# Optimization experiments

Hardware: AMD Instinct MI355X
Metric: run time of the kernel (lower is better)

Reference implementation:

```python
import jax, jax.numpy as jnp
import numpy as np

B, T, N, D = 16, 16, 256, 384  # batch, timesteps, patches, feature dim
QDIM = 384                      # query_dim
TEMP = 1.0                      # temperature
TOPK = 16                       # topk_k
EPS = 1e-8


def setup_inputs() -> dict:
    key = jax.random.key(0)
    k1, k2, k3, k4, k5, k6 = jax.random.split(key, 6)
    queries = jax.random.normal(k1, (B, T, QDIM), dtype=jnp.float32)
    patch_features = jax.random.normal(k2, (B, T, N, D), dtype=jnp.float32)
    # encoder.query_input_proj: Linear(query_dim -> D)
    W_in = jax.random.normal(k3, (QDIM, D), dtype=jnp.float32) / np.sqrt(QDIM)
    b_in = jax.random.normal(k4, (D,), dtype=jnp.float32) * 0.01
    # encoder.query_output_proj: Linear(D -> dino_dim)
    W_out = jax.random.normal(k5, (D, QDIM), dtype=jnp.float32) / np.sqrt(D)
    b_out = jax.random.normal(k6, (QDIM,), dtype=jnp.float32) * 0.01
    return {"queries": queries, "patch_features": patch_features,
            "W_in": W_in, "b_in": b_in, "W_out": W_out, "b_out": b_out}


def reference(queries, patch_features, W_in, b_in, W_out, b_out):
    # q_proj: [B,T,D]
    q_proj = jnp.einsum('btq,qd->btd', queries, W_in) + b_in
    # scores: [B,T,N]
    scores = jnp.einsum('btd,btnd->btn', q_proj, patch_features) / TEMP
    attn = jax.nn.softmax(scores, axis=-1)
    # top-k hard mask + renormalize
    k = min(TOPK, N)
    vals, idx = jax.lax.top_k(attn, k)                     # [B,T,k]
    bi = jnp.arange(B)[:, None, None]
    ti = jnp.arange(T)[None, :, None]
    attn_hard = jnp.zeros_like(attn).at[bi, ti, idx].set(vals)
    attn = attn_hard / (attn_hard.sum(axis=-1, keepdims=True) + EPS)
    # weighted sum over patches: [B,T,D]
    out = jnp.einsum('btn,btnd->btd', attn, patch_features)
    out = jnp.einsum('btd,dq->btq', out, W_out) + b_out    # [B,T,QDIM]
    return out
```

## Files before the change

### kernel.cpp

```cpp
#include <hip/hip_runtime.h>
#include <math.h>

#define B_  16
#define T_  16
#define N_  256
#define D_  384
#define Q_  384
#define K_  16
#define BT_ (B_ * T_)

__global__ __launch_bounds__(1024, 4)
void fused_kernel(const float* __restrict__ queries,
                  const float* __restrict__ patch,
                  const float* __restrict__ W_in,
                  const float* __restrict__ b_in,
                  const float* __restrict__ W_out,
                  const float* __restrict__ b_out,
                  float* __restrict__ out)
{
    const int bt   = blockIdx.x;
    const int tid  = threadIdx.x;
    const int lane = tid & 63;
    const int wave = tid >> 6;

    __shared__ __align__(16) float s_q[Q_];
    __shared__ __align__(16) float s_qp[D_];
    __shared__ float s_sc[N_];
    __shared__ int   s_cnt4[N_][4];
    __shared__ float s_red[4];
    __shared__ float s_red2[4][2];
    __shared__ float s_w[K_];
    __shared__ int   s_ix[K_];
    __shared__ float s_part[2 * D_];
    __shared__ float s_od[D_];

    const float* __restrict__ ptile = patch + (size_t)bt * N_ * D_;

    if (tid < Q_) s_q[tid] = queries[(size_t)bt * Q_ + tid];
    __syncthreads();

    const int g  = lane >> 4;
    const int sl = lane & 15;
    const int n0 = wave * 4 + g;

    float4 A[6], Bu[6];

#define LOADROW(dst, it) {                                                     \
        const float* pr = ptile + (size_t)(n0 + (it) * 64) * D_;               \
        _Pragma("unroll")                                                      \
        for (int c = 0; c < 6; ++c)                                            \
            dst[c] = *reinterpret_cast<const float4*>(pr + c * 64 + 4 * sl); }

#define DOTSTORE(src, it) {                                                    \
        float p = 0.f;                                                         \
        _Pragma("unroll")                                                      \
        for (int c = 0; c < 6; ++c)                                            \
            p += src[c].x * qv[c].x + src[c].y * qv[c].y                       \
               + src[c].z * qv[c].z + src[c].w * qv[c].w;                      \
        _Pragma("unroll")                                                      \
        for (int off = 8; off; off >>= 1) p += __shfl_xor(p, off, 16);         \
        if (sl == 0) s_sc[n0 + (it) * 64] = p; }

    LOADROW(A, 0)
    LOADROW(Bu, 1)
    __builtin_amdgcn_sched_barrier(0);

    if (tid < 2 * D_) {
        const int half = tid >= D_;
        const int d    = tid - half * D_;
        const int q0   = half * (Q_ / 2);
        float a0 = 0.f, a1 = 0.f, a2 = 0.f, a3 = 0.f;
        #pragma unroll 4
        for (int q = q0; q < q0 + Q_ / 2; q += 4) {
            a0 += s_q[q]     * W_in[(size_t)(q)     * D_ + d];
            a1 += s_q[q + 1] * W_in[(size_t)(q + 1) * D_ + d];
            a2 += s_q[q + 2] * W_in[(size_t)(q + 2) * D_ + d];
            a3 += s_q[q + 3] * W_in[(size_t)(q + 3) * D_ + d];
        }
        s_part[tid] = (a0 + a1) + (a2 + a3);
    }
    __syncthreads();
    if (tid < D_) s_qp[tid] = s_part[tid] + s_part[tid + D_] + b_in[tid];
    __syncthreads();

    {
        const float4* s_qp4 = reinterpret_cast<const float4*>(s_qp);
        float4 qv[6];
        #pragma unroll
        for (int c = 0; c < 6; ++c) qv[c] = s_qp4[c * 16 + sl];

        DOTSTORE(A, 0)
        LOADROW(A, 2)
        DOTSTORE(Bu, 1)
        LOADROW(Bu, 3)
        DOTSTORE(A, 2)
        DOTSTORE(Bu, 3)
    }
#undef LOADROW
#undef DOTSTORE
    __syncthreads();

    if (tid < N_) {
        float v = s_sc[tid];
        #pragma unroll
        for (int off = 32; off; off >>= 1) v = fmaxf(v, __shfl_xor(v, off));
        if (lane == 0) s_red[wave] = v;
    }
    {
        const int i   = tid >> 2;
        const int sub = tid & 3;
        const float si = s_sc[i];
        int c = 0;
        #pragma unroll 8
        for (int j = sub * 64; j < sub * 64 + 64; ++j) {
            const float sj = s_sc[j];
            c += (int)(sj > si) | ((int)(sj == si) & (int)(j < i));
        }
        s_cnt4[i][sub] = c;
    }
    __syncthreads();

    float e = 0.f;
    int   cnt = N_;
    if (tid < N_) {
        const float mx = fmaxf(fmaxf(s_red[0], s_red[1]), fmaxf(s_red[2], s_red[3]));
        cnt = s_cnt4[tid][0] + s_cnt4[tid][1] + s_cnt4[tid][2] + s_cnt4[tid][3];
        e = __expf(s_sc[tid] - mx);

        float z  = e;
        float sk = (cnt < K_) ? e : 0.f;
        #pragma unroll
        for (int off = 32; off; off >>= 1) {
            z  += __shfl_xor(z, off);
            sk += __shfl_xor(sk, off);
        }
        if (lane == 0) { s_red2[wave][0] = z; s_red2[wave][1] = sk; }
    }
    __syncthreads();

    {
        const float Z  = s_red2[0][0] + s_red2[1][0] + s_red2[2][0] + s_red2[3][0];
        const float SK = s_red2[0][1] + s_red2[1][1] + s_red2[2][1] + s_red2[3][1];
        const float inv = 1.f / (SK + 1e-8f * Z);
        if (tid < N_ && cnt < K_) {
            s_ix[cnt] = tid;
            s_w[cnt]  = e * inv;
        }
    }
    __syncthreads();

    if (tid < 2 * D_) {
        const int half = tid >= D_;
        const int d    = tid - half * D_;
        const int j0   = half * (K_ / 2);
        float acc = 0.f;
        #pragma unroll
        for (int j = j0; j < j0 + K_ / 2; ++j)
            acc += s_w[j] * ptile[(size_t)s_ix[j] * D_ + d];
        s_part[tid] = acc;
    }
    __syncthreads();
    if (tid < D_) s_od[tid] = s_part[tid] + s_part[tid + D_];
    __syncthreads();

    if (tid < 2 * Q_) {
        const int half = tid >= Q_;
        const int q    = tid - half * Q_;
        const int d0   = half * (D_ / 2);
        float a0 = 0.f, a1 = 0.f, a2 = 0.f, a3 = 0.f;
        #pragma unroll 4
        for (int d = d0; d < d0 + D_ / 2; d += 4) {
            a0 += s_od[d]     * W_out[(size_t)(d)     * Q_ + q];
            a1 += s_od[d + 1] * W_out[(size_t)(d + 1) * Q_ + q];
            a2 += s_od[d + 2] * W_out[(size_t)(d + 2) * Q_ + q];
            a3 += s_od[d + 3] * W_out[(size_t)(d + 3) * Q_ + q];
        }
        s_part[tid] = (a0 + a1) + (a2 + a3);
    }
    __syncthreads();
    if (tid < Q_)
        out[(size_t)bt * Q_ + tid] = s_part[tid] + s_part[tid + Q_] + b_out[tid];
}

extern "C" void kernel_launch(void* const* d_in, const int* in_sizes, int n_in,
                              void* d_out, int out_size, void* d_ws, size_t ws_size,
                              hipStream_t stream) {
    const float* queries = (const float*)d_in[0];
    const float* patch   = (const float*)d_in[1];
    const float* W_in    = (const float*)d_in[2];
    const float* b_in    = (const float*)d_in[3];
    const float* W_out   = (const float*)d_in[4];
    const float* b_out   = (const float*)d_in[5];
    float* out = (float*)d_out;

    fused_kernel<<<dim3(BT_), dim3(1024), 0, stream>>>(
        queries, patch, W_in, b_in, W_out, b_out, out);
}
```

Baseline: 35.95 us.

## Vectorize projection GEMVs with float4 loads and 8-way split-K; vectorize rank counting

Both small matrix-vector products (query input projection and output projection) are restructured so that each thread loads float4 columns of the weight matrix and covers 48 rows, with 8 partial sums per output reduced through shared memory. This replaces the scalar strided loads and the 2-way split. The top-k rank counting loop now reads scores as float4, with a per-sub-group rotation intended to avoid LDS bank conflicts, and the four partial counts are read back as one int4. The cost is a larger shared partial buffer and an 8-term final reduction.

New measurement: 35.67 us. Within noise of the previous version (-0.8%).

```diff
diff --git a/kernel.cpp b/kernel.cpp
--- a/kernel.cpp
+++ b/kernel.cpp
@@ -25,23 +25,24 @@
 
     __shared__ __align__(16) float s_q[Q_];
     __shared__ __align__(16) float s_qp[D_];
-    __shared__ float s_sc[N_];
-    __shared__ int   s_cnt4[N_][4];
+    __shared__ __align__(16) float s_sc[N_];
+    __shared__ __align__(16) int   s_cnt4[N_][4];
     __shared__ float s_red[4];
     __shared__ float s_red2[4][2];
     __shared__ float s_w[K_];
     __shared__ int   s_ix[K_];
-    __shared__ float s_part[2 * D_];
-    __shared__ float s_od[D_];
+    __shared__ __align__(16) float s_p8[8][D_];
+    __shared__ __align__(16) float s_od[D_];
 
     const float* __restrict__ ptile = patch + (size_t)bt * N_ * D_;
+    float* s_flat = &s_p8[0][0];
 
     if (tid < Q_) s_q[tid] = queries[(size_t)bt * Q_ + tid];
     __syncthreads();
 
-    const int g  = lane >> 4;
-    const int sl = lane & 15;
-    const int n0 = wave * 4 + g;
+    const int g16 = lane >> 4;
+    const int sl  = lane & 15;
+    const int n0  = wave * 4 + g16;
 
     float4 A[6], Bu[6];
 
@@ -65,22 +66,27 @@
     LOADROW(Bu, 1)
     __builtin_amdgcn_sched_barrier(0);
 
-    if (tid < 2 * D_) {
-        const int half = tid >= D_;
-        const int d    = tid - half * D_;
-        const int q0   = half * (Q_ / 2);
-        float a0 = 0.f, a1 = 0.f, a2 = 0.f, a3 = 0.f;
+    if (tid < 768) {
+        const int s = tid / 96;
+        const int g = tid % 96;
+        float4 acc = {0.f, 0.f, 0.f, 0.f};
+        const float* wp = W_in + (size_t)(s * 48) * D_ + 4 * g;
         #pragma unroll 4
-        for (int q = q0; q < q0 + Q_ / 2; q += 4) {
-            a0 += s_q[q]     * W_in[(size_t)(q)     * D_ + d];
-            a1 += s_q[q + 1] * W_in[(size_t)(q + 1) * D_ + d];
-            a2 += s_q[q + 2] * W_in[(size_t)(q + 2) * D_ + d];
-            a3 += s_q[q + 3] * W_in[(size_t)(q + 3) * D_ + d];
-        }
-        s_part[tid] = (a0 + a1) + (a2 + a3);
-    }
-    __syncthreads();
-    if (tid < D_) s_qp[tid] = s_part[tid] + s_part[tid + D_] + b_in[tid];
+        for (int qq = 0; qq < 48; ++qq) {
+            const float4 w = *reinterpret_cast<const float4*>(wp + (size_t)qq * D_);
+            const float qs = s_q[s * 48 + qq];
+            acc.x += qs * w.x; acc.y += qs * w.y;
+            acc.z += qs * w.z; acc.w += qs * w.w;
+        }
+        *reinterpret_cast<float4*>(&s_p8[s][4 * g]) = acc;
+    }
+    __syncthreads();
+    if (tid < D_) {
+        float v = b_in[tid];
+        #pragma unroll
+        for (int s = 0; s < 8; ++s) v += s_p8[s][tid];
+        s_qp[tid] = v;
+    }
     __syncthreads();
 
     {
@@ -110,11 +116,17 @@
         const int i   = tid >> 2;
         const int sub = tid & 3;
         const float si = s_sc[i];
+        const float4* s_sc4 = reinterpret_cast<const float4*>(s_sc);
         int c = 0;
-        #pragma unroll 8
-        for (int j = sub * 64; j < sub * 64 + 64; ++j) {
-            const float sj = s_sc[j];
-            c += (int)(sj > si) | ((int)(sj == si) & (int)(j < i));
+        #pragma unroll
+        for (int jj = 0; jj < 16; ++jj) {
+            const int jr = (jj + sub * 4) & 15;
+            const float4 v = s_sc4[sub * 16 + jr];
+            const int j0 = sub * 64 + jr * 4;
+            c += (int)(v.x > si) | ((int)(v.x == si) & (int)((j0 + 0) < i));
+            c += (int)(v.y > si) | ((int)(v.y == si) & (int)((j0 + 1) < i));
+            c += (int)(v.z > si) | ((int)(v.z == si) & (int)((j0 + 2) < i));
+            c += (int)(v.w > si) | ((int)(v.w == si) & (int)((j0 + 3) < i));
         }
         s_cnt4[i][sub] = c;
     }
@@ -124,7 +136,8 @@
     int   cnt = N_;
     if (tid < N_) {
         const float mx = fmaxf(fmaxf(s_red[0], s_red[1]), fmaxf(s_red[2], s_red[3]));
-        cnt = s_cnt4[tid][0] + s_cnt4[tid][1] + s_cnt4[tid][2] + s_cnt4[tid][3];
+        const int4 c4 = reinterpret_cast<const int4*>(s_cnt4)[tid];
+        cnt = c4.x + c4.y + c4.z + c4.w;
         e = __expf(s_sc[tid] - mx);
 
         float z  = e;
@@ -157,29 +170,33 @@
         #pragma unroll
         for (int j = j0; j < j0 + K_ / 2; ++j)
             acc += s_w[j] * ptile[(size_t)s_ix[j] * D_ + d];
-        s_part[tid] = acc;
-    }
-    __syncthreads();
-    if (tid < D_) s_od[tid] = s_part[tid] + s_part[tid + D_];
-    __syncthreads();
-
-    if (tid < 2 * Q_) {
-        const int half = tid >= Q_;
-        const int q    = tid - half * Q_;
-        const int d0   = half * (D_ / 2);
-        float a0 = 0.f, a1 = 0.f, a2 = 0.f, a3 = 0.f;
+        s_flat[tid] = acc;
+    }
+    __syncthreads();
+    if (tid < D_) s_od[tid] = s_flat[tid] + s_flat[tid + D_];
+    __syncthreads();
+
+    if (tid < 768) {
+        const int s = tid / 96;
+        const int g = tid % 96;
+        float4 acc = {0.f, 0.f, 0.f, 0.f};
+        const float* wp = W_out + (size_t)(s * 48) * Q_ + 4 * g;
         #pragma unroll 4
-        for (int d = d0; d < d0 + D_ / 2; d += 4) {
-            a0 += s_od[d]     * W_out[(size_t)(d)     * Q_ + q];
-            a1 += s_od[d + 1] * W_out[(size_t)(d + 1) * Q_ + q];
-            a2 += s_od[d + 2] * W_out[(size_t)(d + 2) * Q_ + q];
-            a3 += s_od[d + 3] * W_out[(size_t)(d + 3) * Q_ + q];
-        }
-        s_part[tid] = (a0 + a1) + (a2 + a3);
-    }
-    __syncthreads();
-    if (tid < Q_)
-        out[(size_t)bt * Q_ + tid] = s_part[tid] + s_part[tid + Q_] + b_out[tid];
+        for (int dd = 0; dd < 48; ++dd) {
+            const float4 w = *reinterpret_cast<const float4*>(wp + (size_t)dd * Q_);
+            const float ov = s_od[s * 48 + dd];
+            acc.x += ov * w.x; acc.y += ov * w.y;
+            acc.z += ov * w.z; acc.w += ov * w.w;
+        }
+        *reinterpret_cast<float4*>(&s_p8[s][4 * g]) = acc;
+    }
+    __syncthreads();
+    if (tid < Q_) {
+        float v = b_out[tid];
+        #pragma unroll
+        for (int s = 0; s < 8; ++s) v += s_p8[s][tid];
+        out[(size_t)bt * Q_ + tid] = v;
+    }
 }
 
 extern "C" void kernel_launch(void* const* d_in, const int* in_sizes, int n_in,
```
